# Optimization experiments

Hardware: AMD Instinct MI355X
Metric: run time of the kernel (lower is better)

## Reference

```python
import jax, jax.numpy as jnp
import numpy as np

DT = 0.02
Z_DIM = 32
U_DIM = 16


def _mlp(x, layers):
    # layers: list of (W, b); SiLU between all but last layer
    n = len(layers)
    for i, (W, b) in enumerate(layers):
        x = x @ W + b
        if i < n - 1:
            x = jax.nn.silu(x)
    return x


def _forward(x, u,
             e_w1, e_b1, e_w2, e_b2, e_w3, e_b3,
             d_w1, d_b1, d_w2, d_b2, d_w3, d_b3, d_w4, d_b4,
             a_w1, a_b1, a_w2, a_b2, a_w3, a_b3,
             b_w1, b_b1, b_w2, b_b2, b_w3, b_b3):
    # encode
    z = _mlp(x, [(e_w1, e_b1), (e_w2, e_b2), (e_w3, e_b3)])          # (B, Z)
    # state-dependent A(x) parameters: pairs (a_i, b_i) per 2x2 block
    aux = _mlp(x, [(a_w1, a_b1), (a_w2, a_b2), (a_w3, a_b3)])        # (B, Z)
    a = aux[:, 0::2]                                                  # (B, Z/2)
    b = aux[:, 1::2]
    f = jnp.exp(a * DT)
    c = jnp.cos(b * DT)
    s = jnp.sin(b * DT)
    # A(x) @ z without materializing block-diagonal: per-pair rotation-scale
    z0 = z[:, 0::2]
    z1 = z[:, 1::2]
    Az = jnp.stack([f * (c * z0 - s * z1), f * (s * z0 + c * z1)], axis=-1).reshape(z.shape)
    # B(x) @ u
    Bmat = _mlp(x, [(b_w1, b_b1), (b_w2, b_b2), (b_w3, b_b3)]).reshape(-1, Z_DIM, U_DIM)
    Bu = jnp.einsum('bzu,bu->bz', Bmat, u)
    # latent Euler step + decode
    z_next = z + DT * (Az + Bu)
    return _mlp(z_next, [(d_w1, d_b1), (d_w2, d_b2), (d_w3, d_b3), (d_w4, d_b4)])


def setup_inputs() -> dict:
    key = jax.random.key(0)
    ks = iter(jax.random.split(key, 32))
    def w(shape, scale=0.02):
        return jax.random.normal(next(ks), shape, jnp.float32) * scale
    B, X, U, Z, H, A = 16384, 64, 16, 32, 1024, 256
    return {
        'x': jax.random.normal(next(ks), (B, X), jnp.float32),
        'u': jax.random.normal(next(ks), (B, U), jnp.float32),
        'e_w1': w((X, H)), 'e_b1': w((H,)),
        'e_w2': w((H, H)), 'e_b2': w((H,)),
        'e_w3': w((H, Z)), 'e_b3': w((Z,)),
        'd_w1': w((Z, H)), 'd_b1': w((H,)),
        'd_w2': w((H, H)), 'd_b2': w((H,)),
        'd_w3': w((H, H)), 'd_b3': w((H,)),
        'd_w4': w((H, X)), 'd_b4': w((X,)),
        'a_w1': w((X, A)), 'a_b1': w((A,)),
        'a_w2': w((A, A)), 'a_b2': w((A,)),
        'a_w3': w((A, Z)), 'a_b3': w((Z,)),
        'b_w1': w((X, A)), 'b_b1': w((A,)),
        'b_w2': w((A, A)), 'b_b2': w((A,)),
        'b_w3': w((A, Z * U)), 'b_b3': w((Z * U,)),
    }


def reference(x, u,
              e_w1, e_b1, e_w2, e_b2, e_w3, e_b3,
              d_w1, d_b1, d_w2, d_b2, d_w3, d_b3, d_w4, d_b4,
              a_w1, a_b1, a_w2, a_b2, a_w3, a_b3,
              b_w1, b_b1, b_w2, b_b2, b_w3, b_b3):
    return _forward(x, u,
                    e_w1, e_b1, e_w2, e_b2, e_w3, e_b3,
                    d_w1, d_b1, d_w2, d_b2, d_w3, d_b3, d_w4, d_b4,
                    a_w1, a_b1, a_w2, a_b2, a_w3, a_b3,
                    b_w1, b_b1, b_w2, b_b2, b_w3, b_b3)
```

## Files before the change

### kernel.cpp

```cpp
#include <hip/hip_runtime.h>
#include <cstdint>
#include <cstddef>

#define B_SZ 16384
#define X_D  64
#define U_D  16
#define Z_D  32
#define H_D  1024
#define A_D  256
#define DT_C 0.02f

typedef _Float16 f16;
typedef f16   f16x8 __attribute__((ext_vector_type(8)));
typedef f16   f16x4 __attribute__((ext_vector_type(4)));
typedef float f32x4 __attribute__((ext_vector_type(4)));

#define AS1 __attribute__((address_space(1)))
#define AS3 __attribute__((address_space(3)))

__device__ __forceinline__ void gld_lds16(const void* g, void* l) {
    __builtin_amdgcn_global_load_lds((AS1 void*)(g), (AS3 void*)(l), 16, 0, 0);
}

template<int BM, int BN, int BK, int WM, int WN, bool SILU, bool OUT16>
__launch_bounds__(256)
__global__ void gemm_f16(const f16* __restrict__ A, const f16* __restrict__ Bt,
                         const float* __restrict__ bias, void* __restrict__ Cp,
                         int M, int N, int K)
{
    constexpr int SEGROW = BK / 8;
    constexpr int SMASK  = (SEGROW < 8 ? SEGROW : 8) - 1;
    constexpr int WTM = BM / WM, WTN = BN / WN;
    constexpr int RM = WTM / 16, RN = WTN / 16;
    constexpr int ITA = (BM * SEGROW) / 256;
    constexpr int ITB = (BN * SEGROW) / 256;

    __shared__ f16 As[BM * BK];
    __shared__ f16 Bs[BN * BK];

    const int tid  = threadIdx.x;
    const int lane = tid & 63;
    const int wave = tid >> 6;
    const int wm = wave / WN, wn = wave % WN;
    const int l15 = lane & 15, quad = lane >> 4;

    const size_t arow0 = (size_t)blockIdx.x * BM;
    const size_t brow0 = (size_t)blockIdx.y * BN;

    f32x4 zero = {0.f, 0.f, 0.f, 0.f};
    f32x4 acc[RM][RN];
#pragma unroll
    for (int i = 0; i < RM; ++i)
#pragma unroll
        for (int j = 0; j < RN; ++j) acc[i][j] = zero;

    for (int k0 = 0; k0 < K; k0 += BK) {
#pragma unroll
        for (int it = 0; it < ITA; ++it) {
            int s = it * 256 + tid;
            int row = s / SEGROW, st = s % SEGROW;
            int sg = st ^ (row & SMASK);
            gld_lds16(A + (arow0 + row) * K + k0 + sg * 8, &As[s * 8]);
        }
#pragma unroll
        for (int it = 0; it < ITB; ++it) {
            int s = it * 256 + tid;
            int row = s / SEGROW, st = s % SEGROW;
            int sg = st ^ (row & SMASK);
            gld_lds16(Bt + (brow0 + row) * K + k0 + sg * 8, &Bs[s * 8]);
        }
        __syncthreads();

#pragma unroll
        for (int kk = 0; kk < BK; kk += 32) {
            f16x8 af[RM], bf[RN];
#pragma unroll
            for (int i = 0; i < RM; ++i) {
                int row = wm * WTM + i * 16 + l15;
                int st  = ((kk >> 3) + quad) ^ (row & SMASK);
                af[i] = *(const f16x8*)&As[(row * SEGROW + st) * 8];
            }
#pragma unroll
            for (int j = 0; j < RN; ++j) {
                int row = wn * WTN + j * 16 + l15;
                int st  = ((kk >> 3) + quad) ^ (row & SMASK);
                bf[j] = *(const f16x8*)&Bs[(row * SEGROW + st) * 8];
            }
#pragma unroll
            for (int i = 0; i < RM; ++i)
#pragma unroll
                for (int j = 0; j < RN; ++j)
                    acc[i][j] = __builtin_amdgcn_mfma_f32_16x16x32_f16(
                        af[i], bf[j], acc[i][j], 0, 0, 0);
        }
        __syncthreads();
    }

    const int rowb = (int)arow0 + wm * WTM;
    const int colb = (int)brow0 + wn * WTN;
#pragma unroll
    for (int j = 0; j < RN; ++j) {
        int col = colb + j * 16 + l15;
        float bv = bias[col];
#pragma unroll
        for (int i = 0; i < RM; ++i) {
#pragma unroll
            for (int r = 0; r < 4; ++r) {
                int row = rowb + i * 16 + quad * 4 + r;
                float v = acc[i][j][r] + bv;
                if (SILU) v = v * (1.0f / (1.0f + __expf(-v)));
                if (OUT16) ((f16*)Cp)[(size_t)row * N + col] = (f16)v;
                else       ((float*)Cp)[(size_t)row * N + col] = v;
            }
        }
    }
}

__global__ void transpose_w_f16(const float* __restrict__ in, f16* __restrict__ out,
                                int K, int N)
{
    __shared__ float t[32][33];
    int n0 = blockIdx.x << 5, k0 = blockIdx.y << 5;
    int tx = threadIdx.x, ty = threadIdx.y;
#pragma unroll
    for (int i = 0; i < 32; i += 8)
        t[ty + i][tx] = in[(size_t)(k0 + ty + i) * N + n0 + tx];
    __syncthreads();
#pragma unroll
    for (int i = 0; i < 32; i += 8)
        out[(size_t)(n0 + ty + i) * K + k0 + tx] = (f16)t[tx][ty + i];
}

__global__ void cvt_f32_f16(const float* __restrict__ in, f16* __restrict__ out)
{
    int i = (blockIdx.x * 256 + threadIdx.x) * 4;
    float4 v = *(const float4*)(in + i);
    f16x4 o = { (f16)v.x, (f16)v.y, (f16)v.z, (f16)v.w };
    *(f16x4*)(out + i) = o;
}

__global__ void koopman_k(const float* __restrict__ zf, const float* __restrict__ auxf,
                          const f16* __restrict__ bmat, const float* __restrict__ u,
                          f16* __restrict__ zn)
{
    int idx = blockIdx.x * 256 + threadIdx.x;
    int i = idx >> 5, zi = idx & 31;
    int base = (i << 5) + ((zi >> 1) << 1);
    float a = auxf[base], b = auxf[base + 1];
    float f = __expf(a * DT_C);
    float c = __cosf(b * DT_C);
    float s = __sinf(b * DT_C);
    float z0 = zf[base], z1 = zf[base + 1];
    float Az = (zi & 1) ? f * (s * z0 + c * z1) : f * (c * z0 - s * z1);
    const f16*   br = bmat + ((size_t)idx << 4);
    const float* ur = u + ((size_t)i << 4);
    float Bu = 0.f;
#pragma unroll
    for (int k = 0; k < 16; ++k) Bu += (float)br[k] * ur[k];
    zn[idx] = (f16)(zf[idx] + DT_C * (Az + Bu));
}

extern "C" void kernel_launch(void* const* d_in, const int* in_sizes, int n_in,
                              void* d_out, int out_size, void* d_ws, size_t ws_size,
                              hipStream_t stream)
{
    (void)in_sizes; (void)n_in; (void)out_size; (void)ws_size;
    const float* x    = (const float*)d_in[0];
    const float* u    = (const float*)d_in[1];
    const float* e_w1 = (const float*)d_in[2];  const float* e_b1 = (const float*)d_in[3];
    const float* e_w2 = (const float*)d_in[4];  const float* e_b2 = (const float*)d_in[5];
    const float* e_w3 = (const float*)d_in[6];  const float* e_b3 = (const float*)d_in[7];
    const float* d_w1 = (const float*)d_in[8];  const float* d_b1 = (const float*)d_in[9];
    const float* d_w2 = (const float*)d_in[10]; const float* d_b2 = (const float*)d_in[11];
    const float* d_w3 = (const float*)d_in[12]; const float* d_b3 = (const float*)d_in[13];
    const float* d_w4 = (const float*)d_in[14]; const float* d_b4 = (const float*)d_in[15];
    const float* a_w1 = (const float*)d_in[16]; const float* a_b1 = (const float*)d_in[17];
    const float* a_w2 = (const float*)d_in[18]; const float* a_b2 = (const float*)d_in[19];
    const float* a_w3 = (const float*)d_in[20]; const float* a_b3 = (const float*)d_in[21];
    const float* b_w1 = (const float*)d_in[22]; const float* b_b1 = (const float*)d_in[23];
    const float* b_w2 = (const float*)d_in[24]; const float* b_b2 = (const float*)d_in[25];
    const float* b_w3 = (const float*)d_in[26]; const float* b_b3 = (const float*)d_in[27];

    char* p = (char*)d_ws;
    auto alloc = [&](size_t nbytes) -> void* {
        void* r = (void*)p;
        p += (nbytes + 255) & ~(size_t)255;
        return r;
    };
    f16*   xb   = (f16*)  alloc((size_t)B_SZ * X_D * 2);
    f16*   h1   = (f16*)  alloc((size_t)B_SZ * H_D * 2);
    f16*   h2   = (f16*)  alloc((size_t)B_SZ * H_D * 2);
    float* zf   = (float*)alloc((size_t)B_SZ * Z_D * 4);
    float* auxf = (float*)alloc((size_t)B_SZ * Z_D * 4);
    f16*   p1   = (f16*)  alloc((size_t)B_SZ * A_D * 2);
    f16*   p2   = (f16*)  alloc((size_t)B_SZ * A_D * 2);
    f16*   bmat = (f16*)  alloc((size_t)B_SZ * (Z_D * U_D) * 2);
    f16*   znb  = (f16*)  alloc((size_t)B_SZ * Z_D * 2);
    f16* e_w1t = (f16*)alloc((size_t)H_D * X_D * 2);
    f16* e_w2t = (f16*)alloc((size_t)H_D * H_D * 2);
    f16* e_w3t = (f16*)alloc((size_t)Z_D * H_D * 2);
    f16* d_w1t = (f16*)alloc((size_t)H_D * Z_D * 2);
    f16* d_w2t = (f16*)alloc((size_t)H_D * H_D * 2);
    f16* d_w3t = (f16*)alloc((size_t)H_D * H_D * 2);
    f16* d_w4t = (f16*)alloc((size_t)X_D * H_D * 2);
    f16* a_w1t = (f16*)alloc((size_t)A_D * X_D * 2);
    f16* a_w2t = (f16*)alloc((size_t)A_D * A_D * 2);
    f16* a_w3t = (f16*)alloc((size_t)Z_D * A_D * 2);
    f16* b_w1t = (f16*)alloc((size_t)A_D * X_D * 2);
    f16* b_w2t = (f16*)alloc((size_t)A_D * A_D * 2);
    f16* b_w3t = (f16*)alloc((size_t)(Z_D * U_D) * A_D * 2);

    dim3 tb(32, 8);
    auto T = [&](const float* w, f16* wt, int K, int N) {
        transpose_w_f16<<<dim3(N / 32, K / 32), tb, 0, stream>>>(w, wt, K, N);
    };
    T(e_w1, e_w1t, X_D, H_D);
    T(e_w2, e_w2t, H_D, H_D);
    T(e_w3, e_w3t, H_D, Z_D);
    T(d_w1, d_w1t, Z_D, H_D);
    T(d_w2, d_w2t, H_D, H_D);
    T(d_w3, d_w3t, H_D, H_D);
    T(d_w4, d_w4t, H_D, X_D);
    T(a_w1, a_w1t, X_D, A_D);
    T(a_w2, a_w2t, A_D, A_D);
    T(a_w3, a_w3t, A_D, Z_D);
    T(b_w1, b_w1t, X_D, A_D);
    T(b_w2, b_w2t, A_D, A_D);
    T(b_w3, b_w3t, A_D, Z_D * U_D);

    cvt_f32_f16<<<(B_SZ * X_D) / 1024, 256, 0, stream>>>(x, xb);

    gemm_f16<128,128,64,2,2,true, true ><<<dim3(B_SZ/128, H_D/128), 256, 0, stream>>>(
        xb, e_w1t, e_b1, h1, B_SZ, H_D, X_D);
    gemm_f16<128,128,64,2,2,true, true ><<<dim3(B_SZ/128, H_D/128), 256, 0, stream>>>(
        h1, e_w2t, e_b2, h2, B_SZ, H_D, H_D);
    gemm_f16<64,32,64,4,1,false,false><<<dim3(B_SZ/64, 1), 256, 0, stream>>>(
        h2, e_w3t, e_b3, zf, B_SZ, Z_D, H_D);
    gemm_f16<128,128,64,2,2,true, true ><<<dim3(B_SZ/128, A_D/128), 256, 0, stream>>>(
        xb, a_w1t, a_b1, p1, B_SZ, A_D, X_D);
    gemm_f16<128,128,64,2,2,true, true ><<<dim3(B_SZ/128, A_D/128), 256, 0, stream>>>(
        p1, a_w2t, a_b2, p2, B_SZ, A_D, A_D);
    gemm_f16<64,32,64,4,1,false,false><<<dim3(B_SZ/64, 1), 256, 0, stream>>>(
        p2, a_w3t, a_b3, auxf, B_SZ, Z_D, A_D);
    gemm_f16<128,128,64,2,2,true, true ><<<dim3(B_SZ/128, A_D/128), 256, 0, stream>>>(
        xb, b_w1t, b_b1, p1, B_SZ, A_D, X_D);
    gemm_f16<128,128,64,2,2,true, true ><<<dim3(B_SZ/128, A_D/128), 256, 0, stream>>>(
        p1, b_w2t, b_b2, p2, B_SZ, A_D, A_D);
    gemm_f16<128,128,64,2,2,false,true ><<<dim3(B_SZ/128, (Z_D*U_D)/128), 256, 0, stream>>>(
        p2, b_w3t, b_b3, bmat, B_SZ, Z_D * U_D, A_D);
    koopman_k<<<(B_SZ * Z_D) / 256, 256, 0, stream>>>(zf, auxf, bmat, u, znb);
    gemm_f16<128,128,32,2,2,true, true ><<<dim3(B_SZ/128, H_D/128), 256, 0, stream>>>(
        znb, d_w1t, d_b1, h1, B_SZ, H_D, Z_D);
    gemm_f16<128,128,64,2,2,true, true ><<<dim3(B_SZ/128, H_D/128), 256, 0, stream>>>(
        h1, d_w2t, d_b2, h2, B_SZ, H_D, H_D);
    gemm_f16<128,128,64,2,2,true, true ><<<dim3(B_SZ/128, H_D/128), 256, 0, stream>>>(
        h2, d_w3t, d_b3, h1, B_SZ, H_D, H_D);
    gemm_f16<64,64,64,2,2,false,false><<<dim3(B_SZ/64, 1), 256, 0, stream>>>(
        h1, d_w4t, d_b4, (float*)d_out, B_SZ, X_D, H_D);
}
```

Baseline: 406.3 us.

## Batch first-layer GEMMs, fuse B(x)u into GEMM epilogue, LDS-staged stores

```diff
diff --git a/kernel.cpp b/kernel.cpp
--- a/kernel.cpp
+++ b/kernel.cpp
@@ -22,12 +22,23 @@
     __builtin_amdgcn_global_load_lds((AS1 void*)(g), (AS3 void*)(l), 16, 0, 0);
 }
 
-template<int BM, int BN, int BK, int WM, int WN, bool SILU, bool OUT16>
+struct GArg {
+    const f16*  A;
+    const f16*  W;
+    const float* bias;
+    void*       C;
+    const float* U;
+    int lda, ldc, K;
+};
+struct GPair { GArg g[2]; };
+
+template<int BM,int BN,int BK,int WM,int WN,bool SILU,int OM>
 __launch_bounds__(256)
-__global__ void gemm_f16(const f16* __restrict__ A, const f16* __restrict__ Bt,
-                         const float* __restrict__ bias, void* __restrict__ Cp,
-                         int M, int N, int K)
+__global__ void gemm_k(GPair p)
 {
+    static_assert(OM != 1 || BN == 128, "OM1 repack assumes BN=128");
+    const GArg ga = p.g[blockIdx.z];
+
     constexpr int SEGROW = BK / 8;
     constexpr int SMASK  = (SEGROW < 8 ? SEGROW : 8) - 1;
     constexpr int WTM = BM / WM, WTN = BN / WN;
@@ -35,8 +46,12 @@
     constexpr int ITA = (BM * SEGROW) / 256;
     constexpr int ITB = (BN * SEGROW) / 256;
 
-    __shared__ f16 As[BM * BK];
-    __shared__ f16 Bs[BN * BK];
+    constexpr int STAGE_B = (BM + BN) * BK * 2;
+    constexpr int CS_B    = (OM == 1) ? BM * BN * 2 : 0;
+    constexpr int SMEM_B  = STAGE_B > CS_B ? STAGE_B : CS_B;
+    __shared__ __align__(16) char smem[SMEM_B];
+    f16* As = (f16*)smem;
+    f16* Bs = As + BM * BK;
 
     const int tid  = threadIdx.x;
     const int lane = tid & 63;
@@ -46,6 +61,7 @@
 
     const size_t arow0 = (size_t)blockIdx.x * BM;
     const size_t brow0 = (size_t)blockIdx.y * BN;
+    const int lda = ga.lda, K = ga.K;
 
     f32x4 zero = {0.f, 0.f, 0.f, 0.f};
     f32x4 acc[RM][RN];
@@ -60,14 +76,14 @@
             int s = it * 256 + tid;
             int row = s / SEGROW, st = s % SEGROW;
             int sg = st ^ (row & SMASK);
-            gld_lds16(A + (arow0 + row) * K + k0 + sg * 8, &As[s * 8]);
+            gld_lds16(ga.A + (arow0 + row) * lda + k0 + sg * 8, &As[s * 8]);
         }
 #pragma unroll
         for (int it = 0; it < ITB; ++it) {
             int s = it * 256 + tid;
             int row = s / SEGROW, st = s % SEGROW;
             int sg = st ^ (row & SMASK);
-            gld_lds16(Bt + (brow0 + row) * K + k0 + sg * 8, &Bs[s * 8]);
+            gld_lds16(ga.W + (brow0 + row) * K + k0 + sg * 8, &Bs[s * 8]);
         }
         __syncthreads();
 
@@ -96,68 +112,140 @@
         __syncthreads();
     }
 
-    const int rowb = (int)arow0 + wm * WTM;
-    const int colb = (int)brow0 + wn * WTN;
-#pragma unroll
-    for (int j = 0; j < RN; ++j) {
-        int col = colb + j * 16 + l15;
-        float bv = bias[col];
+    const int rowbL = wm * WTM;
+    const int colbL = wn * WTN;
+
+    if constexpr (OM == 2) {
+        const int zcol0 = ((int)brow0 + colbL) >> 4;
 #pragma unroll
         for (int i = 0; i < RM; ++i) {
 #pragma unroll
             for (int r = 0; r < 4; ++r) {
-                int row = rowb + i * 16 + quad * 4 + r;
-                float v = acc[i][j][r] + bv;
-                if (SILU) v = v * (1.0f / (1.0f + __expf(-v)));
-                if (OUT16) ((f16*)Cp)[(size_t)row * N + col] = (f16)v;
-                else       ((float*)Cp)[(size_t)row * N + col] = v;
+                int row = (int)arow0 + rowbL + i * 16 + quad * 4 + r;
+                float uv = ga.U[row * 16 + l15];
+#pragma unroll
+                for (int j = 0; j < RN; ++j) {
+                    int col = (int)brow0 + colbL + j * 16 + l15;
+                    float v = (acc[i][j][r] + ga.bias[col]) * uv;
+                    v += __shfl_xor(v, 8, 16);
+                    v += __shfl_xor(v, 4, 16);
+                    v += __shfl_xor(v, 2, 16);
+                    v += __shfl_xor(v, 1, 16);
+                    if (l15 == 0) ((float*)ga.C)[row * 32 + zcol0 + j] = v;
+                }
+            }
+        }
+    } else if constexpr (OM == 1) {
+        f16* Cs = (f16*)smem;
+#pragma unroll
+        for (int j = 0; j < RN; ++j) {
+            int colL = colbL + j * 16 + l15;
+            float bv = ga.bias[(int)brow0 + colL];
+            int chL = colL >> 3, wi = colL & 7;
+#pragma unroll
+            for (int i = 0; i < RM; ++i) {
+#pragma unroll
+                for (int r = 0; r < 4; ++r) {
+                    int rowL = rowbL + i * 16 + quad * 4 + r;
+                    float v = acc[i][j][r] + bv;
+                    if (SILU) v = v / (1.0f + __expf(-v));
+                    Cs[rowL * BN + ((chL ^ (rowL & 15)) << 3) + wi] = (f16)v;
+                }
+            }
+        }
+        __syncthreads();
+        f16* Cout = (f16*)ga.C;
+#pragma unroll
+        for (int pass = 0; pass < (BM * BN / 8) / 256; ++pass) {
+            int s = pass * 256 + tid;
+            int rowL = s >> 4;
+            int ch = s & 15;
+            f16x8 v = *(const f16x8*)&Cs[rowL * BN + ((ch ^ (rowL & 15)) << 3)];
+            *(f16x8*)&Cout[(size_t)(arow0 + rowL) * ga.ldc + brow0 + ch * 8] = v;
+        }
+    } else {
+        float* Cout = (float*)ga.C;
+#pragma unroll
+        for (int j = 0; j < RN; ++j) {
+            int col = (int)brow0 + colbL + j * 16 + l15;
+            float bv = ga.bias[col];
+#pragma unroll
+            for (int i = 0; i < RM; ++i) {
+#pragma unroll
+                for (int r = 0; r < 4; ++r) {
+                    int row = (int)arow0 + rowbL + i * 16 + quad * 4 + r;
+                    float v = acc[i][j][r] + bv;
+                    if (SILU) v = v / (1.0f + __expf(-v));
+                    Cout[(size_t)row * ga.ldc + col] = v;
+                }
             }
         }
     }
 }
 
-__global__ void transpose_w_f16(const float* __restrict__ in, f16* __restrict__ out,
-                                int K, int N)
+struct PrepArgs {
+    const float* w[13];
+    f16*         wt[13];
+    int          K[13];
+    int          N[13];
+    const float* bsrc[3];
+    float*       bias1;
+    const float* x;
+    f16*         xb;
+};
+
+__launch_bounds__(256)
+__global__ void prep_k(PrepArgs pa, int ntrans, int ncvt)
 {
-    __shared__ float t[32][33];
-    int n0 = blockIdx.x << 5, k0 = blockIdx.y << 5;
-    int tx = threadIdx.x, ty = threadIdx.y;
-#pragma unroll
-    for (int i = 0; i < 32; i += 8)
-        t[ty + i][tx] = in[(size_t)(k0 + ty + i) * N + n0 + tx];
-    __syncthreads();
-#pragma unroll
-    for (int i = 0; i < 32; i += 8)
-        out[(size_t)(n0 + ty + i) * K + k0 + tx] = (f16)t[tx][ty + i];
-}
-
-__global__ void cvt_f32_f16(const float* __restrict__ in, f16* __restrict__ out)
-{
-    int i = (blockIdx.x * 256 + threadIdx.x) * 4;
-    float4 v = *(const float4*)(in + i);
-    f16x4 o = { (f16)v.x, (f16)v.y, (f16)v.z, (f16)v.w };
-    *(f16x4*)(out + i) = o;
+    int bid = blockIdx.x;
+    if (bid < ntrans) {
+        int i = 0, t;
+        for (;; ++i) {
+            t = (pa.K[i] >> 5) * (pa.N[i] >> 5);
+            if (bid < t) break;
+            bid -= t;
+        }
+        const int K = pa.K[i], N = pa.N[i];
+        const int tn = N >> 5;
+        const int k0 = (bid / tn) << 5, n0 = (bid % tn) << 5;
+        __shared__ float tbuf[32][33];
+        const int tx = threadIdx.x & 31, ty = threadIdx.x >> 5;
+        const float* src = pa.w[i];
+        f16* dst = pa.wt[i];
+#pragma unroll
+        for (int r = 0; r < 32; r += 8)
+            tbuf[ty + r][tx] = src[(size_t)(k0 + ty + r) * N + n0 + tx];
+        __syncthreads();
+#pragma unroll
+        for (int r = 0; r < 32; r += 8)
+            dst[(size_t)(n0 + ty + r) * K + k0 + tx] = (f16)tbuf[tx][ty + r];
+    } else if (bid < ntrans + ncvt) {
+        int i = ((bid - ntrans) * 256 + threadIdx.x) * 4;
+        float4 v = *(const float4*)(pa.x + i);
+        f16x4 o = {(f16)v.x, (f16)v.y, (f16)v.z, (f16)v.w};
+        *(f16x4*)(pa.xb + i) = o;
+    } else {
+        int idx = (bid - ntrans - ncvt) * 256 + (int)threadIdx.x;
+        float v = (idx < 1024) ? pa.bsrc[0][idx]
+                : (idx < 1280) ? pa.bsrc[1][idx - 1024]
+                               : pa.bsrc[2][idx - 1280];
+        pa.bias1[idx] = v;
+    }
 }
 
 __global__ void koopman_k(const float* __restrict__ zf, const float* __restrict__ auxf,
-                          const f16* __restrict__ bmat, const float* __restrict__ u,
-                          f16* __restrict__ zn)
+                          const float* __restrict__ Buf, f16* __restrict__ zn)
 {
     int idx = blockIdx.x * 256 + threadIdx.x;
-    int i = idx >> 5, zi = idx & 31;
-    int base = (i << 5) + ((zi >> 1) << 1);
+    int zi = idx & 31;
+    int base = idx & ~1;
     float a = auxf[base], b = auxf[base + 1];
     float f = __expf(a * DT_C);
     float c = __cosf(b * DT_C);
     float s = __sinf(b * DT_C);
     float z0 = zf[base], z1 = zf[base + 1];
     float Az = (zi & 1) ? f * (s * z0 + c * z1) : f * (c * z0 - s * z1);
-    const f16*   br = bmat + ((size_t)idx << 4);
-    const float* ur = u + ((size_t)i << 4);
-    float Bu = 0.f;
-#pragma unroll
-    for (int k = 0; k < 16; ++k) Bu += (float)br[k] * ur[k];
-    zn[idx] = (f16)(zf[idx] + DT_C * (Az + Bu));
+    zn[idx] = (f16)(zf[idx] + DT_C * (Az + Buf[idx]));
 }
 
 extern "C" void kernel_launch(void* const* d_in, const int* in_sizes, int n_in,
@@ -188,73 +276,81 @@
         return r;
     };
     f16*   xb   = (f16*)  alloc((size_t)B_SZ * X_D * 2);
-    f16*   h1   = (f16*)  alloc((size_t)B_SZ * H_D * 2);
-    f16*   h2   = (f16*)  alloc((size_t)B_SZ * H_D * 2);
+    f16*   cc1  = (f16*)  alloc((size_t)B_SZ * 1536 * 2);
+    f16*   cc2  = (f16*)  alloc((size_t)B_SZ * 1536 * 2);
     float* zf   = (float*)alloc((size_t)B_SZ * Z_D * 4);
     float* auxf = (float*)alloc((size_t)B_SZ * Z_D * 4);
-    f16*   p1   = (f16*)  alloc((size_t)B_SZ * A_D * 2);
-    f16*   p2   = (f16*)  alloc((size_t)B_SZ * A_D * 2);
-    f16*   bmat = (f16*)  alloc((size_t)B_SZ * (Z_D * U_D) * 2);
+    float* Buf  = (float*)alloc((size_t)B_SZ * Z_D * 4);
     f16*   znb  = (f16*)  alloc((size_t)B_SZ * Z_D * 2);
-    f16* e_w1t = (f16*)alloc((size_t)H_D * X_D * 2);
+    f16*   h1d  = cc1;
+    f16*   h2d  = cc2;
+    f16*   h3d  = cc1;
+    f16*   W1t   = (f16*)alloc((size_t)1536 * X_D * 2);
+    float* bias1 = (float*)alloc(1536 * 4);
     f16* e_w2t = (f16*)alloc((size_t)H_D * H_D * 2);
     f16* e_w3t = (f16*)alloc((size_t)Z_D * H_D * 2);
     f16* d_w1t = (f16*)alloc((size_t)H_D * Z_D * 2);
     f16* d_w2t = (f16*)alloc((size_t)H_D * H_D * 2);
     f16* d_w3t = (f16*)alloc((size_t)H_D * H_D * 2);
     f16* d_w4t = (f16*)alloc((size_t)X_D * H_D * 2);
-    f16* a_w1t = (f16*)alloc((size_t)A_D * X_D * 2);
     f16* a_w2t = (f16*)alloc((size_t)A_D * A_D * 2);
     f16* a_w3t = (f16*)alloc((size_t)Z_D * A_D * 2);
-    f16* b_w1t = (f16*)alloc((size_t)A_D * X_D * 2);
     f16* b_w2t = (f16*)alloc((size_t)A_D * A_D * 2);
     f16* b_w3t = (f16*)alloc((size_t)(Z_D * U_D) * A_D * 2);
 
-    dim3 tb(32, 8);
-    auto T = [&](const float* w, f16* wt, int K, int N) {
-        transpose_w_f16<<<dim3(N / 32, K / 32), tb, 0, stream>>>(w, wt, K, N);
+    PrepArgs pa;
+    const float* ws_[13] = {e_w1, e_w2, e_w3, d_w1, d_w2, d_w3, d_w4,
+                            a_w1, a_w2, a_w3, b_w1, b_w2, b_w3};
+    f16* wts_[13] = {W1t, e_w2t, e_w3t, d_w1t, d_w2t, d_w3t, d_w4t,
+                     W1t + (size_t)1024 * X_D, a_w2t, a_w3t,
+                     W1t + (size_t)1280 * X_D, b_w2t, b_w3t};
+    int Ks_[13] = {X_D, H_D, H_D, Z_D, H_D, H_D, H_D, X_D, A_D, A_D, X_D, A_D, A_D};
+    int Ns_[13] = {H_D, H_D, Z_D, H_D, H_D, H_D, X_D, A_D, A_D, Z_D, A_D, A_D, Z_D*U_D};
+    int ntrans = 0;
+    for (int i = 0; i < 13; ++i) {
+        pa.w[i] = ws_[i]; pa.wt[i] = wts_[i]; pa.K[i] = Ks_[i]; pa.N[i] = Ns_[i];
+        ntrans += (Ks_[i] >> 5) * (Ns_[i] >> 5);
+    }
+    pa.bsrc[0] = e_b1; pa.bsrc[1] = a_b1; pa.bsrc[2] = b_b1;
+    pa.bias1 = bias1; pa.x = x; pa.xb = xb;
+    const int ncvt = (B_SZ * X_D) / 1024;
+    prep_k<<<ntrans + ncvt + 6, 256, 0, stream>>>(pa, ntrans, ncvt);
+
+    auto G = [](const f16* A, const f16* W, const float* bias, void* C,
+                int lda, int ldc, int K, const float* U = nullptr) {
+        GArg g; g.A = A; g.W = W; g.bias = bias; g.C = C; g.U = U;
+        g.lda = lda; g.ldc = ldc; g.K = K; return g;
     };
-    T(e_w1, e_w1t, X_D, H_D);
-    T(e_w2, e_w2t, H_D, H_D);
-    T(e_w3, e_w3t, H_D, Z_D);
-    T(d_w1, d_w1t, Z_D, H_D);
-    T(d_w2, d_w2t, H_D, H_D);
-    T(d_w3, d_w3t, H_D, H_D);
-    T(d_w4, d_w4t, H_D, X_D);
-    T(a_w1, a_w1t, X_D, A_D);
-    T(a_w2, a_w2t, A_D, A_D);
-    T(a_w3, a_w3t, A_D, Z_D);
-    T(b_w1, b_w1t, X_D, A_D);
-    T(b_w2, b_w2t, A_D, A_D);
-    T(b_w3, b_w3t, A_D, Z_D * U_D);
-
-    cvt_f32_f16<<<(B_SZ * X_D) / 1024, 256, 0, stream>>>(x, xb);
-
-    gemm_f16<128,128,64,2,2,true, true ><<<dim3(B_SZ/128, H_D/128), 256, 0, stream>>>(
-        xb, e_w1t, e_b1, h1, B_SZ, H_D, X_D);
-    gemm_f16<128,128,64,2,2,true, true ><<<dim3(B_SZ/128, H_D/128), 256, 0, stream>>>(
-        h1, e_w2t, e_b2, h2, B_SZ, H_D, H_D);
-    gemm_f16<64,32,64,4,1,false,false><<<dim3(B_SZ/64, 1), 256, 0, stream>>>(
-        h2, e_w3t, e_b3, zf, B_SZ, Z_D, H_D);
-    gemm_f16<128,128,64,2,2,true, true ><<<dim3(B_SZ/128, A_D/128), 256, 0, stream>>>(
-        xb, a_w1t, a_b1, p1, B_SZ, A_D, X_D);
-    gemm_f16<128,128,64,2,2,true, true ><<<dim3(B_SZ/128, A_D/128), 256, 0, stream>>>(
-        p1, a_w2t, a_b2, p2, B_SZ, A_D, A_D);
-    gemm_f16<64,32,64,4,1,false,false><<<dim3(B_SZ/64, 1), 256, 0, stream>>>(
-        p2, a_w3t, a_b3, auxf, B_SZ, Z_D, A_D);
-    gemm_f16<128,128,64,2,2,true, true ><<<dim3(B_SZ/128, A_D/128), 256, 0, stream>>>(
-        xb, b_w1t, b_b1, p1, B_SZ, A_D, X_D);
-    gemm_f16<128,128,64,2,2,true, true ><<<dim3(B_SZ/128, A_D/128), 256, 0, stream>>>(
-        p1, b_w2t, b_b2, p2, B_SZ, A_D, A_D);
-    gemm_f16<128,128,64,2,2,false,true ><<<dim3(B_SZ/128, (Z_D*U_D)/128), 256, 0, stream>>>(
-        p2, b_w3t, b_b3, bmat, B_SZ, Z_D * U_D, A_D);
-    koopman_k<<<(B_SZ * Z_D) / 256, 256, 0, stream>>>(zf, auxf, bmat, u, znb);
-    gemm_f16<128,128,32,2,2,true, true ><<<dim3(B_SZ/128, H_D/128), 256, 0, stream>>>(
-        znb, d_w1t, d_b1, h1, B_SZ, H_D, Z_D);
-    gemm_f16<128,128,64,2,2,true, true ><<<dim3(B_SZ/128, H_D/128), 256, 0, stream>>>(
-        h1, d_w2t, d_b2, h2, B_SZ, H_D, H_D);
-    gemm_f16<128,128,64,2,2,true, true ><<<dim3(B_SZ/128, H_D/128), 256, 0, stream>>>(
-        h2, d_w3t, d_b3, h1, B_SZ, H_D, H_D);
-    gemm_f16<64,64,64,2,2,false,false><<<dim3(B_SZ/64, 1), 256, 0, stream>>>(
-        h1, d_w4t, d_b4, (float*)d_out, B_SZ, X_D, H_D);
-}
+    GPair pr;
+
+    pr.g[0] = pr.g[1] = G(xb, W1t, bias1, cc1, X_D, 1536, X_D);
+    gemm_k<128,128,64,2,2,true,1><<<dim3(B_SZ/128, 1536/128, 1), 256, 0, stream>>>(pr);
+
+    pr.g[0] = pr.g[1] = G(cc1, e_w2t, e_b2, cc2, 1536, 1536, H_D);
+    gemm_k<128,128,64,2,2,true,1><<<dim3(B_SZ/128, H_D/128, 1), 256, 0, stream>>>(pr);
+
+    pr.g[0] = G(cc1 + 1024, a_w2t, a_b2, cc2 + 1024, 1536, 1536, A_D);
+    pr.g[1] = G(cc1 + 1280, b_w2t, b_b2, cc2 + 1280, 1536, 1536, A_D);
+    gemm_k<128,128,64,2,2,true,1><<<dim3(B_SZ/128, A_D/128, 2), 256, 0, stream>>>(pr);
+
+    pr.g[0] = G(cc2,        e_w3t, e_b3, zf,   1536, Z_D, H_D);
+    pr.g[1] = G(cc2 + 1024, a_w3t, a_b3, auxf, 1536, Z_D, A_D);
+    gemm_k<64,32,64,4,1,false,0><<<dim3(B_SZ/64, 1, 2), 256, 0, stream>>>(pr);
+
+    pr.g[0] = pr.g[1] = G(cc2 + 1280, b_w3t, b_b3, Buf, 1536, Z_D, A_D, u);
+    gemm_k<128,128,64,2,2,false,2><<<dim3(B_SZ/128, (Z_D*U_D)/128, 1), 256, 0, stream>>>(pr);
+
+    koopman_k<<<(B_SZ * Z_D) / 256, 256, 0, stream>>>(zf, auxf, Buf, znb);
+
+    pr.g[0] = pr.g[1] = G(znb, d_w1t, d_b1, h1d, Z_D, H_D, Z_D);
+    gemm_k<128,128,32,2,2,true,1><<<dim3(B_SZ/128, H_D/128, 1), 256, 0, stream>>>(pr);
+
+    pr.g[0] = pr.g[1] = G(h1d, d_w2t, d_b2, h2d, H_D, H_D, H_D);
+    gemm_k<128,128,64,2,2,true,1><<<dim3(B_SZ/128, H_D/128, 1), 256, 0, stream>>>(pr);
+
+    pr.g[0] = pr.g[1] = G(h2d, d_w3t, d_b3, h3d, H_D, H_D, H_D);
+    gemm_k<128,128,64,2,2,true,1><<<dim3(B_SZ/128, H_D/128, 1), 256, 0, stream>>>(pr);
+
+    pr.g[0] = pr.g[1] = G(h3d, d_w4t, d_b4, d_out, H_D, X_D, H_D);
+    gemm_k<64,64,64,2,2,false,0><<<dim3(B_SZ/64, 1, 1), 256, 0, stream>>>(pr);
+}
```

Result: faster. 378.6 us (-6.8%).
